# Kernel optimization log

Hardware: AMD Instinct MI355X
Metric: run time of the kernel (lower is better)

Reference implementation:

```python
import jax, jax.numpy as jnp
import numpy as np


def setup_inputs() -> dict:
    key = jax.random.key(0)
    ks = jax.random.split(key, 7)
    B, H, W = 32, 28, 28
    C3, C4 = 1024, 2048
    C = C3 + C4            # 3072
    L1 = 9                 # num_landmarks + 1
    A, NC = 312, 200
    return {
        "l3": jax.random.normal(ks[0], (B, C3, H, W), jnp.float32),
        "l4": jax.random.normal(ks[1], (B, C4, H // 2, W // 2), jnp.float32),
        "conv_w": jax.random.normal(ks[2], (L1, C), jnp.float32) * 0.02,
        "modulation": jnp.ones((1, C, L1), jnp.float32),
        "attr_w": jax.random.normal(ks[3], (A, C), jnp.float32) * 0.02,
        "attr_b": jnp.zeros((A,), jnp.float32),
        "class_w": jax.random.normal(ks[4], (NC, A), jnp.float32) * 0.02,
    }


def reference(l3, l4, conv_w, modulation, attr_w, attr_b, class_w):
    b, c3, h, w = l3.shape
    # F.interpolate(l4, (h, w), mode='bilinear', align_corners=False)
    l4_up = jax.image.resize(l4, (b, l4.shape[1], h, w), method="bilinear")
    x = jnp.concatenate([l4_up, l3], axis=1)            # (b, 3072, h, w)

    # 1x1 conv: ab[b,l,h,w] = sum_c w[l,c] * x[b,c,h,w]
    ab = jnp.einsum("lc,bchw->blhw", conv_w, x)
    b_sq = jnp.sum(x * x, axis=1, keepdims=True)        # (b,1,h,w)
    a_sq = jnp.sum(conv_w, axis=1)[None, :, None, None]  # (1,L+1,1,1)  (matches torch: weight.sum(1), NOT squared)
    maps = jax.nn.softmax(-(b_sq - 2.0 * ab + a_sq), axis=1)  # Softmax2d = softmax over channels

    # (maps[:,None] * x[:,:,None]).mean((-1,-2))  ->  batched GEMM over spatial dim
    all_features = jnp.einsum("blhw,bchw->bcl", maps, x) / (h * w)  # (b, c, L+1)

    mod = all_features * modulation                     # dropout is identity at eval
    # permute(0,2,1)[:, :-1, :].mean(1) == mean over landmark dim excluding background
    mean_features = jnp.mean(mod[:, :, :-1], axis=2)    # (b, c)

    attr_scores = mean_features @ attr_w.T + attr_b      # (b, 312)
    class_scores = attr_scores @ class_w.T               # (b, 200)
    return attr_scores, class_scores, maps, all_features
```

## Files before the change

kernel.cpp:

```cpp
#include <hip/hip_runtime.h>
#include <math.h>

#define B_    32
#define C3_   1024
#define C4_   2048
#define C_    3072
#define P_    784
#define Q_    196
#define L_    9
#define NG_   25088
#define A_    312
#define NC_   200

#define ATTR_OFF  0
#define CLASS_OFF 9984
#define MAPS_OFF  16384
#define AF_OFF    242176

#define ASQ_OFF   0
#define MF_OFF    16
#define PART3_OFF (16 + B_ * C_)
#define Y4P_OFF   (PART3_OFF + 8 * 9 * NG_)
#define Y_OFF     (Y4P_OFF + 32 * 16 * 9 * Q_)
#define MP_OFF    (Y_OFF + 32 * 9 * Q_)

typedef __attribute__((ext_vector_type(8))) short bf16x8;
typedef __attribute__((ext_vector_type(4))) float f32x4;

__device__ __forceinline__ short f2bf(float f) {
    union { float f; unsigned u; } v; v.f = f;
    unsigned r = v.u + 0x7FFFu + ((v.u >> 16) & 1u);
    return (short)(r >> 16);
}

__global__ __launch_bounds__(256) void kA(
        const float* __restrict__ l3, const float* __restrict__ l4,
        const float* __restrict__ conv_w,
        float* __restrict__ part3, float* __restrict__ y4p,
        float* __restrict__ asq) {
    int bid = blockIdx.x;
    int t = threadIdx.x;
    if (bid < 784) {
        int g = (bid % 98) * 256 + t;
        int slab = bid / 98;
        int b = g / P_, p = g % P_;
        int c0 = slab * 128;
        const float* xp = l3 + ((size_t)b * C3_ + c0) * P_ + p;
        float ab[9];
#pragma unroll
        for (int l = 0; l < 9; ++l) ab[l] = 0.f;
        for (int i = 0; i < 128; i += 8) {
            float v[8];
#pragma unroll
            for (int k = 0; k < 8; ++k) v[k] = xp[(size_t)k * P_];
            xp += (size_t)8 * P_;
#pragma unroll
            for (int l = 0; l < 9; ++l) {
                const float4 w0 = *(const float4*)(conv_w + l * C_ + C4_ + c0 + i);
                const float4 w1 = *(const float4*)(conv_w + l * C_ + C4_ + c0 + i + 4);
                ab[l] = fmaf(w0.x, v[0], ab[l]);
                ab[l] = fmaf(w0.y, v[1], ab[l]);
                ab[l] = fmaf(w0.z, v[2], ab[l]);
                ab[l] = fmaf(w0.w, v[3], ab[l]);
                ab[l] = fmaf(w1.x, v[4], ab[l]);
                ab[l] = fmaf(w1.y, v[5], ab[l]);
                ab[l] = fmaf(w1.z, v[6], ab[l]);
                ab[l] = fmaf(w1.w, v[7], ab[l]);
            }
        }
#pragma unroll
        for (int l = 0; l < 9; ++l)
            part3[(size_t)(slab * 9 + l) * NG_ + g] = ab[l];
    } else if (bid < 1296) {
        int idx = bid - 784;
        int b = idx >> 4, grp = idx & 15;
        int c0 = grp * 128;
        if (t < Q_) {
            const float* base = l4 + ((size_t)b * C4_ + c0) * Q_ + t;
            float acc[9];
#pragma unroll
            for (int l = 0; l < 9; ++l) acc[l] = 0.f;
            for (int c = 0; c < 128; c += 8) {
                float v[8];
#pragma unroll
                for (int k = 0; k < 8; ++k) v[k] = base[(size_t)(c + k) * Q_];
#pragma unroll
                for (int l = 0; l < 9; ++l) {
                    const float4 w0 = *(const float4*)(conv_w + l * C_ + c0 + c);
                    const float4 w1 = *(const float4*)(conv_w + l * C_ + c0 + c + 4);
                    acc[l] = fmaf(w0.x, v[0], acc[l]);
                    acc[l] = fmaf(w0.y, v[1], acc[l]);
                    acc[l] = fmaf(w0.z, v[2], acc[l]);
                    acc[l] = fmaf(w0.w, v[3], acc[l]);
                    acc[l] = fmaf(w1.x, v[4], acc[l]);
                    acc[l] = fmaf(w1.y, v[5], acc[l]);
                    acc[l] = fmaf(w1.z, v[6], acc[l]);
                    acc[l] = fmaf(w1.w, v[7], acc[l]);
                }
            }
#pragma unroll
            for (int l = 0; l < 9; ++l)
                y4p[(size_t)((b * 16 + grp) * 9 + l) * Q_ + t] = acc[l];
        }
    } else {
        __shared__ float red[256];
        for (int l = 0; l < L_; ++l) {
            float s = 0.f;
            for (int c = t; c < C_; c += 256) s += conv_w[l * C_ + c];
            red[t] = s; __syncthreads();
            for (int o = 128; o > 0; o >>= 1) {
                if (t < o) red[t] += red[t + o];
                __syncthreads();
            }
            if (t == 0) asq[l] = red[0];
            __syncthreads();
        }
    }
}

__global__ __launch_bounds__(256) void kB(const float* __restrict__ y4p,
                                          float* __restrict__ Y) {
    int tid = blockIdx.x * 256 + threadIdx.x;
    if (tid >= 32 * 9 * Q_) return;
    int b = tid / (9 * Q_);
    int r = tid % (9 * Q_);
    float s = 0.f;
#pragma unroll
    for (int grp = 0; grp < 16; ++grp)
        s += y4p[(size_t)(b * 16 + grp) * (9 * Q_) + r];
    Y[(size_t)b * (9 * Q_) + r] = s;
}

__global__ __launch_bounds__(256) void kC(const float* __restrict__ part3,
                                          const float* __restrict__ Y,
                                          const float* __restrict__ asq,
                                          float* __restrict__ out_maps) {
    int g = blockIdx.x * 256 + threadIdx.x;
    int b = g / P_, p = g % P_;
    int yy = p / 28, xx = p % 28;
    float sy = 0.5f * yy - 0.25f, sx = 0.5f * xx - 0.25f;
    float fyf = floorf(sy), fxf = floorf(sx);
    float fy = sy - fyf, fx = sx - fxf;
    int ya = max(0, (int)fyf), yb = min(13, (int)fyf + 1);
    int xa = max(0, (int)fxf), xb = min(13, (int)fxf + 1);
    int o00 = ya * 14 + xa, o01 = ya * 14 + xb;
    int o10 = yb * 14 + xa, o11 = yb * 14 + xb;
    float w00 = (1.f - fy) * (1.f - fx), w01 = (1.f - fy) * fx;
    float w10 = fy * (1.f - fx),         w11 = fy * fx;
    const float* Yb = Y + (size_t)b * (9 * Q_);
    float v[9];
#pragma unroll
    for (int l = 0; l < 9; ++l) {
        const float* Yl = Yb + l * Q_;
        float ab4 = w00 * Yl[o00] + w01 * Yl[o01] + w10 * Yl[o10] + w11 * Yl[o11];
        float ab3 = 0.f;
#pragma unroll
        for (int sl = 0; sl < 8; ++sl)
            ab3 += part3[(size_t)(sl * 9 + l) * NG_ + g];
        v[l] = 2.f * (ab4 + ab3) - asq[l];
    }
    float m = v[0];
#pragma unroll
    for (int l = 1; l < 9; ++l) m = fmaxf(m, v[l]);
    float sum = 0.f;
#pragma unroll
    for (int l = 0; l < 9; ++l) { v[l] = expf(v[l] - m); sum += v[l]; }
    float inv = 1.f / sum;
#pragma unroll
    for (int l = 0; l < 9; ++l)
        out_maps[(size_t)b * (L_ * P_) + l * P_ + p] = v[l] * inv;
}

__device__ __forceinline__ int adj_taps(int q, int* ys, float* wy) {
    if (q == 0)  { ys[0] = 0;  wy[0] = 1.00f; ys[1] = 1;  wy[1] = 0.75f;
                   ys[2] = 2;  wy[2] = 0.25f; return 3; }
    if (q == 13) { ys[0] = 25; wy[0] = 0.25f; ys[1] = 26; wy[1] = 0.75f;
                   ys[2] = 27; wy[2] = 1.00f; return 3; }
    ys[0] = 2 * q - 1; wy[0] = 0.25f;
    ys[1] = 2 * q;     wy[1] = 0.75f;
    ys[2] = 2 * q + 1; wy[2] = 0.75f;
    ys[3] = 2 * q + 2; wy[3] = 0.25f;
    return 4;
}

__global__ __launch_bounds__(256) void kD(const float* __restrict__ maps,
                                          float* __restrict__ Mp) {
    int tid = blockIdx.x * 256 + threadIdx.x;
    if (tid >= 32 * 9 * Q_) return;
    int b = tid / (9 * Q_);
    int r = tid % (9 * Q_);
    int l = r / Q_, q = r % Q_;
    int qy = q / 14, qx = q % 14;
    int ys[4], xs[4]; float wy[4], wx[4];
    int ny = adj_taps(qy, ys, wy);
    int nx = adj_taps(qx, xs, wx);
    const float* mrow = maps + (size_t)b * (L_ * P_) + l * P_;
    float s = 0.f;
    for (int i = 0; i < ny; ++i) {
        float rs = 0.f;
        for (int j = 0; j < nx; ++j)
            rs = fmaf(wx[j], mrow[ys[i] * 28 + xs[j]], rs);
        s = fmaf(wy[i], rs, s);
    }
    Mp[(size_t)b * (9 * Q_) + r] = s;
}

#define KP3 800
#define KP4 224
#define BROW 808
__global__ __launch_bounds__(256) void kE(
        const float* __restrict__ l3, const float* __restrict__ l4,
        const float* __restrict__ maps, const float* __restrict__ Mp,
        float* __restrict__ out_af) {
    __shared__ short bs[16 * BROW];
    int bid = blockIdx.x;
    int t = threadIdx.x;
    int wave = t >> 6, lane = t & 63;
    int row = lane & 15, quad = lane >> 4;

    int b, K, gcbase;
    const float* xbase;
    if (bid < 512) {
        b = bid >> 4;
        int c0 = (bid & 15) * 64 + wave * 16;
        gcbase = C4_ + c0;
        K = 784;
        xbase = l3 + ((size_t)b * C3_ + c0) * P_;
        const float* src = maps + (size_t)b * (L_ * P_);
        for (int i = t; i < 9 * KP3; i += 256) {
            int l = i / KP3, k = i - l * KP3;
            float v = (k < 784) ? src[l * P_ + k] : 0.f;
            bs[l * BROW + k] = f2bf(v);
        }
    } else {
        int idx = bid - 512;
        b = idx >> 5;
        int c0 = (idx & 31) * 64 + wave * 16;
        gcbase = c0;
        K = 196;
        xbase = l4 + ((size_t)b * C4_ + c0) * Q_;
        const float* src = Mp + (size_t)b * (9 * Q_);
        for (int i = t; i < 9 * KP4; i += 256) {
            int l = i / KP4, k = i - l * KP4;
            float v = (k < 196) ? src[l * Q_ + k] : 0.f;
            bs[l * BROW + k] = f2bf(v);
        }
    }
    __syncthreads();

    const float* xrow = xbase + (size_t)row * K;
    const short* brow = bs + row * BROW;
    f32x4 acc = {0.f, 0.f, 0.f, 0.f};
    int kfull = (K / 32) * 32;
#pragma unroll 4
    for (int k0 = 0; k0 < kfull; k0 += 32) {
        int ka = k0 + quad * 8;
        float4 xa = *(const float4*)(xrow + ka);
        float4 xb = *(const float4*)(xrow + ka + 4);
        bf16x8 a;
        a[0] = f2bf(xa.x); a[1] = f2bf(xa.y); a[2] = f2bf(xa.z); a[3] = f2bf(xa.w);
        a[4] = f2bf(xb.x); a[5] = f2bf(xb.y); a[6] = f2bf(xb.z); a[7] = f2bf(xb.w);
        bf16x8 bv = *(const bf16x8*)(brow + ka);
        acc = __builtin_amdgcn_mfma_f32_16x16x32_bf16(a, bv, acc, 0, 0, 0);
    }
    {
        int ka = kfull + quad * 8;
        bf16x8 a;
#pragma unroll
        for (int j = 0; j < 8; ++j)
            a[j] = f2bf((ka + j < K) ? xrow[ka + j] : 0.f);
        bf16x8 bv = *(const bf16x8*)(brow + ka);
        acc = __builtin_amdgcn_mfma_f32_16x16x32_bf16(a, bv, acc, 0, 0, 0);
    }
    int l = row;
    if (l < 9) {
        size_t base = ((size_t)b * C_ + gcbase + quad * 4) * 9 + l;
#pragma unroll
        for (int r = 0; r < 4; ++r)
            out_af[base + (size_t)r * 9] = acc[r] * (1.f / 784.f);
    }
}

__global__ __launch_bounds__(256) void kMF(const float* __restrict__ af,
                                           const float* __restrict__ mod,
                                           float* __restrict__ mf) {
    int i = blockIdx.x * 256 + threadIdx.x;
    if (i >= B_ * C_) return;
    int c = i % C_;
    const float* a = af + (size_t)i * 9;
    const float* m = mod + (size_t)c * 9;
    float s = 0.f;
#pragma unroll
    for (int l = 0; l < 8; ++l) s = fmaf(a[l], m[l], s);
    mf[i] = s * 0.125f;
}

__global__ __launch_bounds__(256) void kF(
        const float* __restrict__ mf, const float* __restrict__ attr_w,
        const float* __restrict__ attr_b, float* __restrict__ out_attr) {
    int idx = blockIdx.x * 4 + (threadIdx.x >> 6);
    int lane = threadIdx.x & 63;
    int b = idx / A_, a = idx % A_;
    const float4* wr = (const float4*)(attr_w + (size_t)a * C_);
    const float4* mr = (const float4*)(mf + (size_t)b * C_);
    float acc = 0.f;
    for (int j = lane; j < C_ / 4; j += 64) {
        float4 w = wr[j], m = mr[j];
        acc += w.x * m.x + w.y * m.y + w.z * m.z + w.w * m.w;
    }
    acc += __shfl_xor(acc, 1);  acc += __shfl_xor(acc, 2);
    acc += __shfl_xor(acc, 4);  acc += __shfl_xor(acc, 8);
    acc += __shfl_xor(acc, 16); acc += __shfl_xor(acc, 32);
    if (lane == 0) out_attr[idx] = acc + attr_b[a];
}

__global__ __launch_bounds__(256) void kG(
        const float* __restrict__ attr, const float* __restrict__ class_w,
        float* __restrict__ out_class) {
    int idx = blockIdx.x * 4 + (threadIdx.x >> 6);
    int lane = threadIdx.x & 63;
    int b = idx / NC_, n = idx % NC_;
    float acc = 0.f;
    for (int a = lane; a < A_; a += 64)
        acc += attr[b * A_ + a] * class_w[n * A_ + a];
    acc += __shfl_xor(acc, 1);  acc += __shfl_xor(acc, 2);
    acc += __shfl_xor(acc, 4);  acc += __shfl_xor(acc, 8);
    acc += __shfl_xor(acc, 16); acc += __shfl_xor(acc, 32);
    if (lane == 0) out_class[idx] = acc;
}

extern "C" void kernel_launch(void* const* d_in, const int* in_sizes, int n_in,
                              void* d_out, int out_size, void* d_ws, size_t ws_size,
                              hipStream_t stream) {
    (void)in_sizes; (void)n_in; (void)out_size; (void)ws_size;
    const float* l3         = (const float*)d_in[0];
    const float* l4         = (const float*)d_in[1];
    const float* conv_w     = (const float*)d_in[2];
    const float* modulation = (const float*)d_in[3];
    const float* attr_w     = (const float*)d_in[4];
    const float* attr_b     = (const float*)d_in[5];
    const float* class_w    = (const float*)d_in[6];
    float* out = (float*)d_out;
    float* ws  = (float*)d_ws;
    float* asq   = ws + ASQ_OFF;
    float* mf    = ws + MF_OFF;
    float* part3 = ws + PART3_OFF;
    float* y4p   = ws + Y4P_OFF;
    float* Y     = ws + Y_OFF;
    float* Mp    = ws + MP_OFF;

    kA<<<1297, 256, 0, stream>>>(l3, l4, conv_w, part3, y4p, asq);
    kB<<<221, 256, 0, stream>>>(y4p, Y);
    kC<<<98, 256, 0, stream>>>(part3, Y, asq, out + MAPS_OFF);
    kD<<<221, 256, 0, stream>>>(out + MAPS_OFF, Mp);
    kE<<<1536, 256, 0, stream>>>(l3, l4, out + MAPS_OFF, Mp, out + AF_OFF);
    kMF<<<384, 256, 0, stream>>>(out + AF_OFF, modulation, mf);
    kF<<<(B_ * A_) / 4, 256, 0, stream>>>(mf, attr_w, attr_b, out + ATTR_OFF);
    kG<<<(B_ * NC_) / 4, 256, 0, stream>>>(out + ATTR_OFF, class_w,
                                           out + CLASS_OFF);
}
```

Measured before the change: 308.0 us.

## Register-block kA over 4 pixels and stage kE operands through LDS with K-splitting

kA now has each thread compute 4 adjacent pixels using float4 loads over 64-channel slabs. This doubles the number of partial slabs reduced in kB and kC. kE now stages both the feature tile and the maps operand in LDS as bf16 in uniform 196-wide K chunks, splitting the l3 spatial dimension into 4 parts. kMF reduces those 4 partial sums and writes the final features. The aim is wider, coalesced loads and better latency hiding, at the cost of more partial-sum traffic and a shared workspace region (PAF aliases PART3, which is only safe because kC consumes part3 before kE runs).

After: 317.7 us. +3.2%, slower.

```diff
diff --git a/kernel.cpp b/kernel.cpp
--- a/kernel.cpp
+++ b/kernel.cpp
@@ -19,9 +19,10 @@
 
 #define ASQ_OFF   0
 #define MF_OFF    16
-#define PART3_OFF (16 + B_ * C_)
-#define Y4P_OFF   (PART3_OFF + 8 * 9 * NG_)
-#define Y_OFF     (Y4P_OFF + 32 * 16 * 9 * Q_)
+#define PART3_OFF 98320
+#define PAF_OFF   98320
+#define Y4P_OFF   (PART3_OFF + 16 * 9 * NG_)
+#define Y_OFF     (Y4P_OFF + 32 * 32 * 9 * Q_)
 #define MP_OFF    (Y_OFF + 32 * 9 * Q_)
 
 typedef __attribute__((ext_vector_type(8))) short bf16x8;
@@ -40,68 +41,78 @@
         float* __restrict__ asq) {
     int bid = blockIdx.x;
     int t = threadIdx.x;
-    if (bid < 784) {
-        int g = (bid % 98) * 256 + t;
-        int slab = bid / 98;
-        int b = g / P_, p = g % P_;
-        int c0 = slab * 128;
-        const float* xp = l3 + ((size_t)b * C3_ + c0) * P_ + p;
-        float ab[9];
-#pragma unroll
-        for (int l = 0; l < 9; ++l) ab[l] = 0.f;
-        for (int i = 0; i < 128; i += 8) {
-            float v[8];
-#pragma unroll
-            for (int k = 0; k < 8; ++k) v[k] = xp[(size_t)k * P_];
-            xp += (size_t)8 * P_;
+    if (bid < 392) {
+        int tid = bid * 256 + t;
+        int slab = tid / 6272;
+        int rem = tid % 6272;
+        int b = rem / 196, chunk = rem % 196;
+        int px = chunk * 4;
+        int c0 = slab * 64;
+        const float* xp = l3 + ((size_t)b * C3_ + c0) * P_ + px;
+        float ab[9][4];
+#pragma unroll
+        for (int l = 0; l < 9; ++l)
+#pragma unroll
+            for (int j = 0; j < 4; ++j) ab[l][j] = 0.f;
+        for (int c = 0; c < 64; c += 8) {
+            float4 v[8];
+#pragma unroll
+            for (int k = 0; k < 8; ++k)
+                v[k] = *(const float4*)(xp + (size_t)(c + k) * P_);
 #pragma unroll
             for (int l = 0; l < 9; ++l) {
-                const float4 w0 = *(const float4*)(conv_w + l * C_ + C4_ + c0 + i);
-                const float4 w1 = *(const float4*)(conv_w + l * C_ + C4_ + c0 + i + 4);
-                ab[l] = fmaf(w0.x, v[0], ab[l]);
-                ab[l] = fmaf(w0.y, v[1], ab[l]);
-                ab[l] = fmaf(w0.z, v[2], ab[l]);
-                ab[l] = fmaf(w0.w, v[3], ab[l]);
-                ab[l] = fmaf(w1.x, v[4], ab[l]);
-                ab[l] = fmaf(w1.y, v[5], ab[l]);
-                ab[l] = fmaf(w1.z, v[6], ab[l]);
-                ab[l] = fmaf(w1.w, v[7], ab[l]);
-            }
-        }
-#pragma unroll
-        for (int l = 0; l < 9; ++l)
-            part3[(size_t)(slab * 9 + l) * NG_ + g] = ab[l];
-    } else if (bid < 1296) {
-        int idx = bid - 784;
-        int b = idx >> 4, grp = idx & 15;
-        int c0 = grp * 128;
-        if (t < Q_) {
-            const float* base = l4 + ((size_t)b * C4_ + c0) * Q_ + t;
-            float acc[9];
-#pragma unroll
-            for (int l = 0; l < 9; ++l) acc[l] = 0.f;
-            for (int c = 0; c < 128; c += 8) {
-                float v[8];
-#pragma unroll
-                for (int k = 0; k < 8; ++k) v[k] = base[(size_t)(c + k) * Q_];
-#pragma unroll
-                for (int l = 0; l < 9; ++l) {
-                    const float4 w0 = *(const float4*)(conv_w + l * C_ + c0 + c);
-                    const float4 w1 = *(const float4*)(conv_w + l * C_ + c0 + c + 4);
-                    acc[l] = fmaf(w0.x, v[0], acc[l]);
-                    acc[l] = fmaf(w0.y, v[1], acc[l]);
-                    acc[l] = fmaf(w0.z, v[2], acc[l]);
-                    acc[l] = fmaf(w0.w, v[3], acc[l]);
-                    acc[l] = fmaf(w1.x, v[4], acc[l]);
-                    acc[l] = fmaf(w1.y, v[5], acc[l]);
-                    acc[l] = fmaf(w1.z, v[6], acc[l]);
-                    acc[l] = fmaf(w1.w, v[7], acc[l]);
+                const float4 w0 = *(const float4*)(conv_w + l * C_ + C4_ + c0 + c);
+                const float4 w1 = *(const float4*)(conv_w + l * C_ + C4_ + c0 + c + 4);
+                const float wv[8] = {w0.x, w0.y, w0.z, w0.w, w1.x, w1.y, w1.z, w1.w};
+#pragma unroll
+                for (int k = 0; k < 8; ++k) {
+                    ab[l][0] = fmaf(wv[k], v[k].x, ab[l][0]);
+                    ab[l][1] = fmaf(wv[k], v[k].y, ab[l][1]);
+                    ab[l][2] = fmaf(wv[k], v[k].z, ab[l][2]);
+                    ab[l][3] = fmaf(wv[k], v[k].w, ab[l][3]);
                 }
             }
-#pragma unroll
-            for (int l = 0; l < 9; ++l)
-                y4p[(size_t)((b * 16 + grp) * 9 + l) * Q_ + t] = acc[l];
-        }
+        }
+#pragma unroll
+        for (int l = 0; l < 9; ++l)
+            *(float4*)(part3 + (size_t)(slab * 9 + l) * NG_ + b * P_ + px) =
+                make_float4(ab[l][0], ab[l][1], ab[l][2], ab[l][3]);
+    } else if (bid < 588) {
+        int tid = (bid - 392) * 256 + t;
+        int grp = tid / 1568;
+        int rem = tid % 1568;
+        int b = rem / 49, chunk = rem % 49;
+        int q = chunk * 4;
+        int c0 = grp * 64;
+        const float* xp = l4 + ((size_t)b * C4_ + c0) * Q_ + q;
+        float ac[9][4];
+#pragma unroll
+        for (int l = 0; l < 9; ++l)
+#pragma unroll
+            for (int j = 0; j < 4; ++j) ac[l][j] = 0.f;
+        for (int c = 0; c < 64; c += 8) {
+            float4 v[8];
+#pragma unroll
+            for (int k = 0; k < 8; ++k)
+                v[k] = *(const float4*)(xp + (size_t)(c + k) * Q_);
+#pragma unroll
+            for (int l = 0; l < 9; ++l) {
+                const float4 w0 = *(const float4*)(conv_w + l * C_ + c0 + c);
+                const float4 w1 = *(const float4*)(conv_w + l * C_ + c0 + c + 4);
+                const float wv[8] = {w0.x, w0.y, w0.z, w0.w, w1.x, w1.y, w1.z, w1.w};
+#pragma unroll
+                for (int k = 0; k < 8; ++k) {
+                    ac[l][0] = fmaf(wv[k], v[k].x, ac[l][0]);
+                    ac[l][1] = fmaf(wv[k], v[k].y, ac[l][1]);
+                    ac[l][2] = fmaf(wv[k], v[k].z, ac[l][2]);
+                    ac[l][3] = fmaf(wv[k], v[k].w, ac[l][3]);
+                }
+            }
+        }
+#pragma unroll
+        for (int l = 0; l < 9; ++l)
+            *(float4*)(y4p + (size_t)((b * 32 + grp) * 9 + l) * Q_ + q) =
+                make_float4(ac[l][0], ac[l][1], ac[l][2], ac[l][3]);
     } else {
         __shared__ float red[256];
         for (int l = 0; l < L_; ++l) {
@@ -126,8 +137,8 @@
     int r = tid % (9 * Q_);
     float s = 0.f;
 #pragma unroll
-    for (int grp = 0; grp < 16; ++grp)
-        s += y4p[(size_t)(b * 16 + grp) * (9 * Q_) + r];
+    for (int grp = 0; grp < 32; ++grp)
+        s += y4p[(size_t)(b * 32 + grp) * (9 * Q_) + r];
     Y[(size_t)b * (9 * Q_) + r] = s;
 }
 
@@ -155,7 +166,7 @@
         float ab4 = w00 * Yl[o00] + w01 * Yl[o01] + w10 * Yl[o10] + w11 * Yl[o11];
         float ab3 = 0.f;
 #pragma unroll
-        for (int sl = 0; sl < 8; ++sl)
+        for (int sl = 0; sl < 16; ++sl)
             ab3 += part3[(size_t)(sl * 9 + l) * NG_ + g];
         v[l] = 2.f * (ab4 + ab3) - asq[l];
     }
@@ -205,93 +216,118 @@
     Mp[(size_t)b * (9 * Q_) + r] = s;
 }
 
-#define KP3 800
-#define KP4 224
-#define BROW 808
+#define SA 232
 __global__ __launch_bounds__(256) void kE(
         const float* __restrict__ l3, const float* __restrict__ l4,
         const float* __restrict__ maps, const float* __restrict__ Mp,
-        float* __restrict__ out_af) {
-    __shared__ short bs[16 * BROW];
+        float* __restrict__ out_af, float* __restrict__ paf) {
+    __shared__ short As[64 * SA];
+    __shared__ short Bs[16 * SA];
     int bid = blockIdx.x;
     int t = threadIdx.x;
     int wave = t >> 6, lane = t & 63;
-    int row = lane & 15, quad = lane >> 4;
-
-    int b, K, gcbase;
-    const float* xbase;
-    if (bid < 512) {
-        b = bid >> 4;
-        int c0 = (bid & 15) * 64 + wave * 16;
-        gcbase = C4_ + c0;
-        K = 784;
-        xbase = l3 + ((size_t)b * C3_ + c0) * P_;
-        const float* src = maps + (size_t)b * (L_ * P_);
-        for (int i = t; i < 9 * KP3; i += 256) {
-            int l = i / KP3, k = i - l * KP3;
-            float v = (k < 784) ? src[l * P_ + k] : 0.f;
-            bs[l * BROW + k] = f2bf(v);
-        }
+    int row16 = lane & 15, quad = lane >> 4;
+
+    const float* xsrc; size_t xstride;
+    const float* bsrc; size_t bstride;
+    int b, c0, h;
+    bool isl4 = (bid < 1024);
+    if (isl4) {
+        b = bid >> 5;
+        c0 = (bid & 31) * 64;
+        h = 0;
+        xsrc = l4 + ((size_t)b * C4_ + c0) * Q_;
+        xstride = Q_;
+        bsrc = Mp + (size_t)b * (9 * Q_);
+        bstride = Q_;
     } else {
-        int idx = bid - 512;
-        b = idx >> 5;
-        int c0 = (idx & 31) * 64 + wave * 16;
-        gcbase = c0;
-        K = 196;
-        xbase = l4 + ((size_t)b * C4_ + c0) * Q_;
-        const float* src = Mp + (size_t)b * (9 * Q_);
-        for (int i = t; i < 9 * KP4; i += 256) {
-            int l = i / KP4, k = i - l * KP4;
-            float v = (k < 196) ? src[l * Q_ + k] : 0.f;
-            bs[l * BROW + k] = f2bf(v);
-        }
+        int idx = bid - 1024;
+        b = idx >> 6;
+        c0 = ((idx >> 2) & 15) * 64;
+        h = idx & 3;
+        xsrc = l3 + ((size_t)b * C3_ + c0) * P_ + h * Q_;
+        xstride = P_;
+        bsrc = maps + (size_t)b * (L_ * P_) + h * Q_;
+        bstride = P_;
+    }
+
+    for (int i = t; i < 64 * 49; i += 256) {
+        int r = i / 49, j = (i % 49) * 4;
+        float4 v = *(const float4*)(xsrc + (size_t)r * xstride + j);
+        ushort4 o;
+        o.x = (unsigned short)f2bf(v.x); o.y = (unsigned short)f2bf(v.y);
+        o.z = (unsigned short)f2bf(v.z); o.w = (unsigned short)f2bf(v.w);
+        *(ushort4*)(As + r * SA + j) = o;
+    }
+    for (int i = t; i < 64 * 9; i += 256) {
+        int r = i / 9, j = 196 + (i % 9) * 4;
+        *(ushort4*)(As + r * SA + j) = make_ushort4(0, 0, 0, 0);
+    }
+    for (int i = t; i < 16 * 58; i += 256) {
+        int r = i / 58, j = (i % 58) * 4;
+        ushort4 o = make_ushort4(0, 0, 0, 0);
+        if (r < 9 && j < 196) {
+            float4 v = *(const float4*)(bsrc + (size_t)r * bstride + j);
+            o.x = (unsigned short)f2bf(v.x); o.y = (unsigned short)f2bf(v.y);
+            o.z = (unsigned short)f2bf(v.z); o.w = (unsigned short)f2bf(v.w);
+        }
+        *(ushort4*)(Bs + r * SA + j) = o;
     }
     __syncthreads();
 
-    const float* xrow = xbase + (size_t)row * K;
-    const short* brow = bs + row * BROW;
+    const short* arow = As + (wave * 16 + row16) * SA;
+    const short* brow = Bs + row16 * SA;
     f32x4 acc = {0.f, 0.f, 0.f, 0.f};
-    int kfull = (K / 32) * 32;
-#pragma unroll 4
-    for (int k0 = 0; k0 < kfull; k0 += 32) {
-        int ka = k0 + quad * 8;
-        float4 xa = *(const float4*)(xrow + ka);
-        float4 xb = *(const float4*)(xrow + ka + 4);
-        bf16x8 a;
-        a[0] = f2bf(xa.x); a[1] = f2bf(xa.y); a[2] = f2bf(xa.z); a[3] = f2bf(xa.w);
-        a[4] = f2bf(xb.x); a[5] = f2bf(xb.y); a[6] = f2bf(xb.z); a[7] = f2bf(xb.w);
-        bf16x8 bv = *(const bf16x8*)(brow + ka);
+#pragma unroll
+    for (int k0 = 0; k0 < 224; k0 += 32) {
+        bf16x8 a = *(const bf16x8*)(arow + k0 + quad * 8);
+        bf16x8 bv = *(const bf16x8*)(brow + k0 + quad * 8);
         acc = __builtin_amdgcn_mfma_f32_16x16x32_bf16(a, bv, acc, 0, 0, 0);
     }
-    {
-        int ka = kfull + quad * 8;
-        bf16x8 a;
-#pragma unroll
-        for (int j = 0; j < 8; ++j)
-            a[j] = f2bf((ka + j < K) ? xrow[ka + j] : 0.f);
-        bf16x8 bv = *(const bf16x8*)(brow + ka);
-        acc = __builtin_amdgcn_mfma_f32_16x16x32_bf16(a, bv, acc, 0, 0, 0);
-    }
-    int l = row;
+    int l = row16;
     if (l < 9) {
-        size_t base = ((size_t)b * C_ + gcbase + quad * 4) * 9 + l;
-#pragma unroll
-        for (int r = 0; r < 4; ++r)
-            out_af[base + (size_t)r * 9] = acc[r] * (1.f / 784.f);
-    }
-}
-
-__global__ __launch_bounds__(256) void kMF(const float* __restrict__ af,
+        int c = c0 + wave * 16 + quad * 4;
+        if (isl4) {
+            size_t base = ((size_t)b * C_ + c) * 9 + l;
+#pragma unroll
+            for (int r = 0; r < 4; ++r)
+                out_af[base + (size_t)r * 9] = acc[r] * (1.f / 784.f);
+        } else {
+            size_t base = ((size_t)(h * B_ + b) * C3_ + c) * 9 + l;
+#pragma unroll
+            for (int r = 0; r < 4; ++r)
+                paf[base + (size_t)r * 9] = acc[r];
+        }
+    }
+}
+
+__global__ __launch_bounds__(256) void kMF(const float* __restrict__ paf,
                                            const float* __restrict__ mod,
+                                           float* __restrict__ out_af,
                                            float* __restrict__ mf) {
     int i = blockIdx.x * 256 + threadIdx.x;
     if (i >= B_ * C_) return;
-    int c = i % C_;
-    const float* a = af + (size_t)i * 9;
+    int b = i / C_, c = i % C_;
+    float af[9];
+    if (c < C4_) {
+#pragma unroll
+        for (int l = 0; l < 9; ++l) af[l] = out_af[(size_t)i * 9 + l];
+    } else {
+        int c3 = c - C4_;
+#pragma unroll
+        for (int l = 0; l < 9; ++l) {
+            float s = 0.f;
+#pragma unroll
+            for (int hh = 0; hh < 4; ++hh)
+                s += paf[((size_t)(hh * B_ + b) * C3_ + c3) * 9 + l];
+            af[l] = s * (1.f / 784.f);
+            out_af[(size_t)i * 9 + l] = af[l];
+        }
+    }
     const float* m = mod + (size_t)c * 9;
     float s = 0.f;
 #pragma unroll
-    for (int l = 0; l < 8; ++l) s = fmaf(a[l], m[l], s);
+    for (int l = 0; l < 8; ++l) s = fmaf(af[l], m[l], s);
     mf[i] = s * 0.125f;
 }
 
@@ -345,16 +381,17 @@
     float* asq   = ws + ASQ_OFF;
     float* mf    = ws + MF_OFF;
     float* part3 = ws + PART3_OFF;
+    float* paf   = ws + PAF_OFF;
     float* y4p   = ws + Y4P_OFF;
     float* Y     = ws + Y_OFF;
     float* Mp    = ws + MP_OFF;
 
-    kA<<<1297, 256, 0, stream>>>(l3, l4, conv_w, part3, y4p, asq);
+    kA<<<589, 256, 0, stream>>>(l3, l4, conv_w, part3, y4p, asq);
     kB<<<221, 256, 0, stream>>>(y4p, Y);
     kC<<<98, 256, 0, stream>>>(part3, Y, asq, out + MAPS_OFF);
     kD<<<221, 256, 0, stream>>>(out + MAPS_OFF, Mp);
-    kE<<<1536, 256, 0, stream>>>(l3, l4, out + MAPS_OFF, Mp, out + AF_OFF);
-    kMF<<<384, 256, 0, stream>>>(out + AF_OFF, modulation, mf);
+    kE<<<3072, 256, 0, stream>>>(l3, l4, out + MAPS_OFF, Mp, out + AF_OFF, paf);
+    kMF<<<384, 256, 0, stream>>>(paf, modulation, out + AF_OFF, mf);
     kF<<<(B_ * A_) / 4, 256, 0, stream>>>(mf, attr_w, attr_b, out + ATTR_OFF);
     kG<<<(B_ * NC_) / 4, 256, 0, stream>>>(out + ATTR_OFF, class_w,
                                            out + CLASS_OFF);
```
